# Kernel tuning notes

Hardware: AMD Instinct MI355X
Metric: run time of the kernel (lower is better)

The kernel has to match this reference:

```python
import jax, jax.numpy as jnp
import numpy as np

FACTOR = 2
EPS = 1e-5


def _layernorm_last(x, w, b):
    # LayerNorm over the last dim only (torch nn.LayerNorm(size) with int size)
    mu = jnp.mean(x, axis=-1, keepdims=True)
    var = jnp.var(x, axis=-1, keepdims=True)
    return (x - mu) * jax.lax.rsqrt(var + EPS) * w + b


def setup_inputs() -> dict:
    key = jax.random.key(0)
    ks = jax.random.split(key, 12)
    B, C, H, W = 8, 512, 128, 128
    C8 = C // 8
    S = (H // FACTOR)  # = 64, LayerNorm size
    x = jax.random.normal(ks[0], (B, C, H, W), jnp.float32)
    s = 1.0 / np.sqrt(C)
    wq = jax.random.normal(ks[1], (C8, C), jnp.float32) * s
    bq = jax.random.normal(ks[2], (C8,), jnp.float32) * 0.02
    wk = jax.random.normal(ks[3], (C8, C), jnp.float32) * s
    bk = jax.random.normal(ks[4], (C8,), jnp.float32) * 0.02
    wv = jax.random.normal(ks[5], (C, C), jnp.float32) * s
    bv = jax.random.normal(ks[6], (C,), jnp.float32) * 0.02
    gamma = jax.random.normal(ks[7], (1,), jnp.float32) * 0.1
    ln_in_w = 1.0 + 0.1 * jax.random.normal(ks[8], (S,), jnp.float32)
    ln_in_b = 0.1 * jax.random.normal(ks[9], (S,), jnp.float32)
    ln_out_w = 1.0 + 0.1 * jax.random.normal(ks[10], (S,), jnp.float32)
    ln_out_b = 0.1 * jax.random.normal(ks[11], (S,), jnp.float32)
    return {"x": x, "wq": wq, "bq": bq, "wk": wk, "bk": bk, "wv": wv, "bv": bv,
            "gamma": gamma, "ln_in_w": ln_in_w, "ln_in_b": ln_in_b,
            "ln_out_w": ln_out_w, "ln_out_b": ln_out_b}


def reference(x, wq, bq, wk, bk, wv, bv, gamma, ln_in_w, ln_in_b, ln_out_w, ln_out_b):
    B, C, H, W = x.shape
    f = FACTOR
    Hp, Wp = H // f, W // f
    N = Hp * Wp
    # AvgPool2d(factor)
    xp = x.reshape(B, C, Hp, f, Wp, f).mean(axis=(3, 5))
    # LayerNorm over last dim (width)
    xn = _layernorm_last(xp, ln_in_w, ln_in_b)
    # 1x1 conv projections (einsum over channels)
    q = jnp.einsum('oc,bchw->bohw', wq, xn) + bq[None, :, None, None]
    k = jnp.einsum('oc,bchw->bohw', wk, xn) + bk[None, :, None, None]
    v = jnp.einsum('oc,bchw->bohw', wv, xn) + bv[None, :, None, None]
    q = q.reshape(B, -1, N)  # (B, C/8, N)
    k = k.reshape(B, -1, N)
    v = v.reshape(B, C, N)
    # energy = Q^T K, no scale (as in source)
    energy = jnp.einsum('bcn,bcm->bnm', q, k)  # (B, N, N)
    att = jax.nn.softmax(energy, axis=-1)
    # out = V @ att^T : out[b,c,n] = sum_m v[b,c,m] * att[b,n,m]
    out = jnp.einsum('bcm,bnm->bcn', v, att).reshape(B, C, Hp, Wp)
    out = _layernorm_last(out, ln_out_w, ln_out_b)
    # F.interpolate(scale_factor=f) -> nearest upsample
    out = jnp.repeat(jnp.repeat(out, f, axis=2), f, axis=3)
    return gamma * out + x
```

## Files before the change

kernel.cpp:

```cpp
#include <hip/hip_runtime.h>
#include <hip/hip_bf16.h>
#include <stdint.h>

#define BB 8
#define CC 512
#define HH 128
#define WW 128
#define HP 64
#define NN 4096
#define C8 64
#define EPSF 1e-5f
#define LOG2E 1.4426950408889634f
#define SM_SHIFT 46.0f

typedef __attribute__((ext_vector_type(8))) short short8;
typedef __attribute__((ext_vector_type(4))) float f32x4;

__device__ __forceinline__ float bf2f(ushort u) {
    union { uint i; float f; } x; x.i = ((uint)u) << 16; return x.f;
}
__device__ __forceinline__ ushort f2bf(float f) {
    uint i = __float_as_uint(f);
    return (ushort)((i + 0x7FFFu + ((i >> 16) & 1u)) >> 16);
}
__device__ __forceinline__ uint cvt_pk_bf16(float lo, float hi) {
    uint r;
    asm("v_cvt_pk_bf16_f32 %0, %1, %2" : "=v"(r) : "v"(lo), "v"(hi));
    return r;
}

__global__ __launch_bounds__(256) void pool_ln_kernel(
    const float* __restrict__ x, const float* __restrict__ lw,
    const float* __restrict__ lb, ushort* __restrict__ xn)
{
    int wid = threadIdx.x >> 6, lane = threadIdx.x & 63;
    int row = blockIdx.x * 4 + wid;
    int h = row & 63;
    int bc = row >> 6;
    const float* r0 = x + ((size_t)bc * 128 + 2 * h) * 128;
    const float* r1 = r0 + 128;
    float2 a0 = ((const float2*)r0)[lane];
    float2 a1 = ((const float2*)r1)[lane];
    float p = 0.25f * (a0.x + a0.y + a1.x + a1.y);
    float s = p, sq = p * p;
    #pragma unroll
    for (int m = 1; m < 64; m <<= 1) {
        s  += __shfl_xor(s,  m, 64);
        sq += __shfl_xor(sq, m, 64);
    }
    float mu  = s * (1.f / 64.f);
    float var = sq * (1.f / 64.f) - mu * mu;
    float inv = rsqrtf(var + EPSF);
    float v = (p - mu) * inv * lw[lane] + lb[lane];
    xn[(size_t)bc * NN + h * 64 + lane] = f2bf(v);
}

__global__ __launch_bounds__(256) void qkv_kernel(
    const ushort* __restrict__ xn,
    const float* __restrict__ wq, const float* __restrict__ bq,
    const float* __restrict__ wk, const float* __restrict__ bk,
    const float* __restrict__ wv, const float* __restrict__ bv,
    ushort* __restrict__ qt, ushort* __restrict__ kt, ushort* __restrict__ vo)
{
    __shared__ __align__(16) ushort As[64][40];
    __shared__ __align__(16) ushort Bs[64][66];
    int b = blockIdx.z, mt = blockIdx.y;
    int n0 = blockIdx.x * 64;
    const float* W; const float* bias;
    if (mt == 0)      { W = wq;                               bias = bq; }
    else if (mt == 1) { W = wk;                               bias = bk; }
    else              { W = wv + (size_t)(mt - 2) * 64 * 512; bias = bv + (mt - 2) * 64; }
    float mult = (mt == 0) ? LOG2E : 1.0f;
    const ushort* xb = xn + (size_t)b * CC * NN;
    int t = threadIdx.x;
    int lane = t & 63, wid = t >> 6;
    int wm = wid >> 1, wn = wid & 1;
    f32x4 acc[2][2] = {};

    for (int kc = 0; kc < 512; kc += 32) {
        {
            int row = t >> 2, k8 = (t & 3) * 8;
            const float* wp_ = &W[row * 512 + kc + k8];
            float4 f0 = *(const float4*)wp_;
            float4 f1 = *(const float4*)(wp_ + 4);
            ushort tmp[8] = { f2bf(f0.x * mult), f2bf(f0.y * mult), f2bf(f0.z * mult), f2bf(f0.w * mult),
                              f2bf(f1.x * mult), f2bf(f1.y * mult), f2bf(f1.z * mult), f2bf(f1.w * mult) };
            *(uint4*)&As[row][k8] = *(const uint4*)tmp;
        }
        {
            int c = t >> 3, n8 = (t & 7) * 8;
            uint4 v = *(const uint4*)&xb[(size_t)(kc + c) * NN + n0 + n8];
            const ushort* pv = (const ushort*)&v;
            #pragma unroll
            for (int e = 0; e < 8; e++) Bs[n8 + e][c] = pv[e];
        }
        __syncthreads();
        short8 a[2];
        #pragma unroll
        for (int fm = 0; fm < 2; fm++)
            a[fm] = *(const short8*)&As[wm * 32 + fm * 16 + (lane & 15)][(lane >> 4) * 8];
        short8 bb[2];
        #pragma unroll
        for (int fn = 0; fn < 2; fn++) {
            int col = wn * 32 + fn * 16 + (lane & 15);
            union { short8 v; uint u[4]; } bu;
            int c0 = (lane >> 4) * 8;
            #pragma unroll
            for (int p = 0; p < 4; p++)
                bu.u[p] = *(const uint*)&Bs[col][c0 + 2 * p];
            bb[fn] = bu.v;
        }
        #pragma unroll
        for (int fm = 0; fm < 2; fm++)
            #pragma unroll
            for (int fn = 0; fn < 2; fn++)
                acc[fm][fn] = __builtin_amdgcn_mfma_f32_16x16x32_bf16(a[fm], bb[fn], acc[fm][fn], 0, 0, 0);
        __syncthreads();
    }
    if (mt <= 1) {
        ushort* ot = ((mt == 0) ? qt : kt) + (size_t)b * NN * 64;
        #pragma unroll
        for (int fm = 0; fm < 2; fm++) {
            #pragma unroll
            for (int fn = 0; fn < 2; fn++) {
                int col = n0 + wn * 32 + fn * 16 + (lane & 15);
                int c0  = wm * 32 + fm * 16 + (lane >> 4) * 4;
                ushort tmp[4];
                #pragma unroll
                for (int r = 0; r < 4; r++)
                    tmp[r] = f2bf(acc[fm][fn][r] + bias[c0 + r] * mult);
                *(uint2*)&ot[(size_t)col * 64 + c0] = *(const uint2*)tmp;
            }
        }
    } else {
        ushort* outp = vo + (size_t)b * CC * NN + (size_t)(mt - 2) * 64 * NN;
        #pragma unroll
        for (int fm = 0; fm < 2; fm++) {
            #pragma unroll
            for (int fn = 0; fn < 2; fn++) {
                int col = n0 + wn * 32 + fn * 16 + (lane & 15);
                #pragma unroll
                for (int r = 0; r < 4; r++) {
                    int orow = wm * 32 + fm * 16 + (lane >> 4) * 4 + r;
                    outp[(size_t)orow * NN + col] = f2bf(acc[fm][fn][r] + bias[orow]);
                }
            }
        }
    }
}

__global__ __launch_bounds__(256, 4) void attn_kernel(
    const ushort* __restrict__ qt, const ushort* __restrict__ ktg,
    const ushort* __restrict__ vg, const float* __restrict__ x,
    const float* __restrict__ gamma_p,
    const float* __restrict__ lnw_g, const float* __restrict__ lnb_g,
    float* __restrict__ out)
{
    __shared__ __align__(16) ushort ktl[2][4096];
    __shared__ __align__(16) ushort Ps[2][64][68];
    __shared__ float row_l[64];
    __shared__ float lnw[64], lnb[64];

    int bid = blockIdx.x;
    int b  = bid & 7;
    int cq = (bid >> 3) & 3;
    int h  = bid >> 5;
    int t = threadIdx.x, wid = t >> 6, lane = t & 63;
    int l15 = lane & 15, hig = lane >> 4;
    const ushort* ktb = ktg + (size_t)b * NN * 64;
    const ushort* vb  = vg  + (size_t)b * CC * NN;

    if (t < 64) { lnw[t] = lnw_g[t]; lnb[t] = lnb_g[t]; }

    const ushort* qrow = qt + (size_t)b * NN * 64 + (size_t)(h * 64 + wid * 16 + l15) * 64;
    short8 qf0 = *(const short8*)&qrow[hig * 8];
    short8 qf1 = *(const short8*)&qrow[32 + hig * 8];

    int s0 = t, s1 = t + 256;
    int sm0 = s0 >> 3, sc0 = s0 & 7;
    int sm1 = s1 >> 3, sc1 = s1 & 7;
    int o0 = sm0 * 64 + ((sc0 ^ (sm0 & 7)) * 8);
    int o1 = sm1 * 64 + ((sc1 ^ (sm1 & 7)) * 8);

    f32x4 acc[4][2] = {};
    float lsum = 0.f;
    int cbase = cq * 128 + wid * 32;
    int nrow = wid * 16 + l15;
    int mq4 = hig * 4;

    const ushort* vp0 = vb + (size_t)(cbase + l15) * NN + hig * 8;
    const ushort* vp1 = vp0 + (size_t)16 * NN;

    {
        uint4 ka = *(const uint4*)(ktb + s0 * 8);
        uint4 kb2 = *(const uint4*)(ktb + s1 * 8);
        *(uint4*)&ktl[0][o0] = ka;
        *(uint4*)&ktl[0][o1] = kb2;
    }
    __syncthreads();

    for (int mt2 = 0; mt2 < 64; mt2++) {
        int cur = mt2 & 1, nxt = cur ^ 1;
        int m0 = mt2 * 64;

        const ushort* ktn = ktb + (size_t)(((mt2 + 1) & 63) * 4096);
        uint4 sa = *(const uint4*)(ktn + s0 * 8);
        uint4 sb = *(const uint4*)(ktn + s1 * 8);
        short8 vreg[4];
        #pragma unroll
        for (int ks = 0; ks < 2; ks++) {
            vreg[ks * 2]     = *(const short8*)(vp0 + m0 + ks * 32);
            vreg[ks * 2 + 1] = *(const short8*)(vp1 + m0 + ks * 32);
        }
        __builtin_amdgcn_sched_barrier(0);

        f32x4 sfT[4];
        #pragma unroll
        for (int mf = 0; mf < 4; mf++) {
            int m = mf * 16 + l15;
            int base = m * 64;
            int k7 = m & 7;
            short8 k0 = *(const short8*)&ktl[cur][base + ((hig ^ k7) * 8)];
            short8 k1 = *(const short8*)&ktl[cur][base + (((hig + 4) ^ k7) * 8)];
            f32x4 s = {};
            s = __builtin_amdgcn_mfma_f32_16x16x32_bf16(k0, qf0, s, 0, 0, 0);
            s = __builtin_amdgcn_mfma_f32_16x16x32_bf16(k1, qf1, s, 0, 0, 0);
            sfT[mf] = s;
        }

        #pragma unroll
        for (int fn = 0; fn < 4; fn++) {
            float e0 = exp2f(sfT[fn][0] - SM_SHIFT);
            float e1 = exp2f(sfT[fn][1] - SM_SHIFT);
            float e2 = exp2f(sfT[fn][2] - SM_SHIFT);
            float e3 = exp2f(sfT[fn][3] - SM_SHIFT);
            lsum += (e0 + e1) + (e2 + e3);
            uint2 pk;
            pk.x = cvt_pk_bf16(e0, e1);
            pk.y = cvt_pk_bf16(e2, e3);
            *(uint2*)&Ps[cur][nrow][fn * 16 + mq4] = pk;
        }

        *(uint4*)&ktl[nxt][o0] = sa;
        *(uint4*)&ktl[nxt][o1] = sb;

        __syncthreads();

        #pragma unroll
        for (int ks = 0; ks < 2; ks++) {
            short8 pa[4];
            #pragma unroll
            for (int f = 0; f < 4; f++)
                pa[f] = *(const short8*)&Ps[cur][f * 16 + l15][ks * 32 + hig * 8];
            #pragma unroll
            for (int g = 0; g < 2; g++)
                #pragma unroll
                for (int f = 0; f < 4; f++)
                    acc[f][g] = __builtin_amdgcn_mfma_f32_16x16x32_bf16(pa[f], vreg[ks * 2 + g], acc[f][g], 0, 0, 0);
        }
    }

    lsum += __shfl_xor(lsum, 16, 64);
    lsum += __shfl_xor(lsum, 32, 64);
    if (lane < 16) row_l[wid * 16 + lane] = lsum;
    __syncthreads();

    float g = gamma_p[0];
    const float* xb2 = x + (size_t)b * CC * HH * WW;
    float* ob = out + (size_t)b * CC * HH * WW;
    float rl[4][4], lwv[4][4], lbv[4][4];
    #pragma unroll
    for (int fm = 0; fm < 4; fm++)
        #pragma unroll
        for (int r = 0; r < 4; r++) {
            int n = fm * 16 + hig * 4 + r;
            rl[fm][r] = 1.f / row_l[n];
            lwv[fm][r] = lnw[n]; lbv[fm][r] = lnb[n];
        }
    #pragma unroll
    for (int fc = 0; fc < 2; fc++) {
        int c = cbase + fc * 16 + l15;
        float vv[4][4];
        float vsum = 0.f, vsq = 0.f;
        #pragma unroll
        for (int fm = 0; fm < 4; fm++)
            #pragma unroll
            for (int r = 0; r < 4; r++) {
                float v = acc[fm][fc][r] * rl[fm][r];
                vv[fm][r] = v; vsum += v; vsq += v * v;
            }
        vsum += __shfl_xor(vsum, 16, 64); vsum += __shfl_xor(vsum, 32, 64);
        vsq  += __shfl_xor(vsq,  16, 64); vsq  += __shfl_xor(vsq,  32, 64);
        float mu  = vsum * (1.f / 64.f);
        float var = vsq * (1.f / 64.f) - mu * mu;
        float inv = rsqrtf(var + EPSF);
        const float* xrow = xb2 + (size_t)c * HH * WW + (2 * h) * WW;
        float*       orow = ob  + (size_t)c * HH * WW + (2 * h) * WW;
        #pragma unroll
        for (int fm = 0; fm < 4; fm++) {
            int nbase = fm * 16 + hig * 4;
            float nv[4];
            #pragma unroll
            for (int r = 0; r < 4; r++)
                nv[r] = g * ((vv[fm][r] - mu) * inv * lwv[fm][r] + lbv[fm][r]);
            #pragma unroll
            for (int dh = 0; dh < 2; dh++) {
                float4 xv0 = *(const float4*)&xrow[dh * WW + 2 * nbase];
                float4 xv1 = *(const float4*)&xrow[dh * WW + 2 * nbase + 4];
                float4 o0, o1;
                o0.x = nv[0] + xv0.x; o0.y = nv[0] + xv0.y;
                o0.z = nv[1] + xv0.z; o0.w = nv[1] + xv0.w;
                o1.x = nv[2] + xv1.x; o1.y = nv[2] + xv1.y;
                o1.z = nv[3] + xv1.z; o1.w = nv[3] + xv1.w;
                *(float4*)&orow[dh * WW + 2 * nbase]     = o0;
                *(float4*)&orow[dh * WW + 2 * nbase + 4] = o1;
            }
        }
    }
}

extern "C" void kernel_launch(void* const* d_in, const int* in_sizes, int n_in,
                              void* d_out, int out_size, void* d_ws, size_t ws_size,
                              hipStream_t stream)
{
    (void)in_sizes; (void)n_in; (void)out_size; (void)ws_size;
    const float* x    = (const float*)d_in[0];
    const float* wq   = (const float*)d_in[1];
    const float* bq   = (const float*)d_in[2];
    const float* wk   = (const float*)d_in[3];
    const float* bk   = (const float*)d_in[4];
    const float* wv   = (const float*)d_in[5];
    const float* bv   = (const float*)d_in[6];
    const float* gam  = (const float*)d_in[7];
    const float* lniw = (const float*)d_in[8];
    const float* lnib = (const float*)d_in[9];
    const float* lnow = (const float*)d_in[10];
    const float* lnob = (const float*)d_in[11];
    float* out = (float*)d_out;

    char* ws = (char*)d_ws;
    ushort* xn = (ushort*)(ws);
    ushort* qt = (ushort*)(ws + 33554432u);
    ushort* kt = (ushort*)(ws + 37748736u);
    ushort* v  = (ushort*)(ws + 41943040u);

    pool_ln_kernel<<<65536, 256, 0, stream>>>(x, lniw, lnib, xn);
    qkv_kernel<<<dim3(64, 10, 8), 256, 0, stream>>>(xn, wq, bq, wk, bk, wv, bv, qt, kt, v);
    attn_kernel<<<2048, 256, 0, stream>>>(qt, kt, v, x, gam, lnow, lnob, out);
}
```

Measured before the change: 495.8 us.

## Cover all channels per attention block with 8 waves to avoid recomputing QK

The attention kernel goes from 4 channel-quarter blocks per query tile to one 512-thread block that covers all 512 channels. Each wave now accumulates 64 channels, and the QK^T/exp work is split across the two wave halves, with the row sums combined through two shared arrays. This removes the fourfold recomputation of scores and softmax and the repeated K tile loads. The cost is a larger accumulator footprint per wave (16 MFMA tiles), more V registers, and only 512 blocks in the grid, which may lower occupancy and latency hiding.

```diff
diff --git a/kernel.cpp b/kernel.cpp
--- a/kernel.cpp
+++ b/kernel.cpp
@@ -149,7 +149,7 @@
     }
 }
 
-__global__ __launch_bounds__(256, 4) void attn_kernel(
+__global__ __launch_bounds__(512, 4) void attn_kernel(
     const ushort* __restrict__ qt, const ushort* __restrict__ ktg,
     const ushort* __restrict__ vg, const float* __restrict__ x,
     const float* __restrict__ gamma_p,
@@ -158,66 +158,50 @@
 {
     __shared__ __align__(16) ushort ktl[2][4096];
     __shared__ __align__(16) ushort Ps[2][64][68];
-    __shared__ float row_l[64];
+    __shared__ float row_lA[64], row_lB[64];
     __shared__ float lnw[64], lnb[64];
 
     int bid = blockIdx.x;
-    int b  = bid & 7;
-    int cq = (bid >> 3) & 3;
-    int h  = bid >> 5;
+    int b = bid & 7;
+    int h = bid >> 3;
     int t = threadIdx.x, wid = t >> 6, lane = t & 63;
     int l15 = lane & 15, hig = lane >> 4;
+    int w3 = wid & 3;
+    int mh = wid >> 2;
     const ushort* ktb = ktg + (size_t)b * NN * 64;
     const ushort* vb  = vg  + (size_t)b * CC * NN;
 
     if (t < 64) { lnw[t] = lnw_g[t]; lnb[t] = lnb_g[t]; }
 
-    const ushort* qrow = qt + (size_t)b * NN * 64 + (size_t)(h * 64 + wid * 16 + l15) * 64;
+    const ushort* qrow = qt + (size_t)b * NN * 64 + (size_t)(h * 64 + w3 * 16 + l15) * 64;
     short8 qf0 = *(const short8*)&qrow[hig * 8];
     short8 qf1 = *(const short8*)&qrow[32 + hig * 8];
 
-    int s0 = t, s1 = t + 256;
-    int sm0 = s0 >> 3, sc0 = s0 & 7;
-    int sm1 = s1 >> 3, sc1 = s1 & 7;
-    int o0 = sm0 * 64 + ((sc0 ^ (sm0 & 7)) * 8);
-    int o1 = sm1 * 64 + ((sc1 ^ (sm1 & 7)) * 8);
-
-    f32x4 acc[4][2] = {};
+    int sm = t >> 3, sc = t & 7;
+    int oo = sm * 64 + ((sc ^ (sm & 7)) * 8);
+
+    f32x4 acc[4][4] = {};
     float lsum = 0.f;
-    int cbase = cq * 128 + wid * 32;
-    int nrow = wid * 16 + l15;
+    int cbase = wid * 64;
+    int nrow = w3 * 16 + l15;
     int mq4 = hig * 4;
 
-    const ushort* vp0 = vb + (size_t)(cbase + l15) * NN + hig * 8;
-    const ushort* vp1 = vp0 + (size_t)16 * NN;
-
-    {
-        uint4 ka = *(const uint4*)(ktb + s0 * 8);
-        uint4 kb2 = *(const uint4*)(ktb + s1 * 8);
-        *(uint4*)&ktl[0][o0] = ka;
-        *(uint4*)&ktl[0][o1] = kb2;
-    }
+    const ushort* vbase = vb + (size_t)(cbase + l15) * NN + hig * 8;
+
+    *(uint4*)&ktl[0][oo] = *(const uint4*)(ktb + t * 8);
     __syncthreads();
 
     for (int mt2 = 0; mt2 < 64; mt2++) {
         int cur = mt2 & 1, nxt = cur ^ 1;
         int m0 = mt2 * 64;
 
-        const ushort* ktn = ktb + (size_t)(((mt2 + 1) & 63) * 4096);
-        uint4 sa = *(const uint4*)(ktn + s0 * 8);
-        uint4 sb = *(const uint4*)(ktn + s1 * 8);
-        short8 vreg[4];
-        #pragma unroll
-        for (int ks = 0; ks < 2; ks++) {
-            vreg[ks * 2]     = *(const short8*)(vp0 + m0 + ks * 32);
-            vreg[ks * 2 + 1] = *(const short8*)(vp1 + m0 + ks * 32);
-        }
+        uint4 sa = *(const uint4*)(ktb + (size_t)(((mt2 + 1) & 63) * 4096) + t * 8);
         __builtin_amdgcn_sched_barrier(0);
 
-        f32x4 sfT[4];
-        #pragma unroll
-        for (int mf = 0; mf < 4; mf++) {
-            int m = mf * 16 + l15;
+        f32x4 sfT[2];
+        #pragma unroll
+        for (int lf = 0; lf < 2; lf++) {
+            int m = (mh * 2 + lf) * 16 + l15;
             int base = m * 64;
             int k7 = m & 7;
             short8 k0 = *(const short8*)&ktl[cur][base + ((hig ^ k7) * 8)];
@@ -225,24 +209,31 @@
             f32x4 s = {};
             s = __builtin_amdgcn_mfma_f32_16x16x32_bf16(k0, qf0, s, 0, 0, 0);
             s = __builtin_amdgcn_mfma_f32_16x16x32_bf16(k1, qf1, s, 0, 0, 0);
-            sfT[mf] = s;
-        }
-
-        #pragma unroll
-        for (int fn = 0; fn < 4; fn++) {
-            float e0 = exp2f(sfT[fn][0] - SM_SHIFT);
-            float e1 = exp2f(sfT[fn][1] - SM_SHIFT);
-            float e2 = exp2f(sfT[fn][2] - SM_SHIFT);
-            float e3 = exp2f(sfT[fn][3] - SM_SHIFT);
+            sfT[lf] = s;
+        }
+
+        #pragma unroll
+        for (int lf = 0; lf < 2; lf++) {
+            float e0 = exp2f(sfT[lf][0] - SM_SHIFT);
+            float e1 = exp2f(sfT[lf][1] - SM_SHIFT);
+            float e2 = exp2f(sfT[lf][2] - SM_SHIFT);
+            float e3 = exp2f(sfT[lf][3] - SM_SHIFT);
             lsum += (e0 + e1) + (e2 + e3);
             uint2 pk;
             pk.x = cvt_pk_bf16(e0, e1);
             pk.y = cvt_pk_bf16(e2, e3);
-            *(uint2*)&Ps[cur][nrow][fn * 16 + mq4] = pk;
-        }
-
-        *(uint4*)&ktl[nxt][o0] = sa;
-        *(uint4*)&ktl[nxt][o1] = sb;
+            *(uint2*)&Ps[cur][nrow][(mh * 2 + lf) * 16 + mq4] = pk;
+        }
+
+        short8 vreg[8];
+        #pragma unroll
+        for (int ks = 0; ks < 2; ks++)
+            #pragma unroll
+            for (int g = 0; g < 4; g++)
+                vreg[ks * 4 + g] = *(const short8*)(vbase + (size_t)g * 16 * NN + m0 + ks * 32);
+
+        *(uint4*)&ktl[nxt][oo] = sa;
+        __builtin_amdgcn_sched_barrier(0);
 
         __syncthreads();
 
@@ -253,16 +244,19 @@
             for (int f = 0; f < 4; f++)
                 pa[f] = *(const short8*)&Ps[cur][f * 16 + l15][ks * 32 + hig * 8];
             #pragma unroll
-            for (int g = 0; g < 2; g++)
+            for (int g = 0; g < 4; g++)
                 #pragma unroll
                 for (int f = 0; f < 4; f++)
-                    acc[f][g] = __builtin_amdgcn_mfma_f32_16x16x32_bf16(pa[f], vreg[ks * 2 + g], acc[f][g], 0, 0, 0);
+                    acc[f][g] = __builtin_amdgcn_mfma_f32_16x16x32_bf16(pa[f], vreg[ks * 4 + g], acc[f][g], 0, 0, 0);
         }
     }
 
     lsum += __shfl_xor(lsum, 16, 64);
     lsum += __shfl_xor(lsum, 32, 64);
-    if (lane < 16) row_l[wid * 16 + lane] = lsum;
+    if (lane < 16) {
+        if (mh == 0) row_lA[w3 * 16 + lane] = lsum;
+        else         row_lB[w3 * 16 + lane] = lsum;
+    }
     __syncthreads();
 
     float g = gamma_p[0];
@@ -274,11 +268,11 @@
         #pragma unroll
         for (int r = 0; r < 4; r++) {
             int n = fm * 16 + hig * 4 + r;
-            rl[fm][r] = 1.f / row_l[n];
+            rl[fm][r] = 1.f / (row_lA[n] + row_lB[n]);
             lwv[fm][r] = lnw[n]; lbv[fm][r] = lnb[n];
         }
     #pragma unroll
-    for (int fc = 0; fc < 2; fc++) {
+    for (int fc = 0; fc < 4; fc++) {
         int c = cbase + fc * 16 + l15;
         float vv[4][4];
         float vsum = 0.f, vsq = 0.f;
@@ -346,5 +340,5 @@
 
     pool_ln_kernel<<<65536, 256, 0, stream>>>(x, lniw, lnib, xn);
     qkv_kernel<<<dim3(64, 10, 8), 256, 0, stream>>>(xn, wq, bq, wk, bk, wv, bv, qt, kt, v);
-    attn_kernel<<<2048, 256, 0, stream>>>(qt, kt, v, x, gam, lnow, lnob, out);
-}
+    attn_kernel<<<512, 512, 0, stream>>>(qt, kt, v, x, gam, lnow, lnob, out);
+}
```

Result: slower. 593.5 us (+19.7%).
